# Kernel tuning notes

Hardware: AMD Instinct MI355X
Metric: run time of the kernel (lower is better)

Reference implementation:

```python
import jax, jax.numpy as jnp
import numpy as np

N = 40000
E = 640000
IN = 1300
H = 4
C = 64
G = 64  # number of graphs in the batch
NEG_SLOPE = 0.2


def gat_conv(x, edge_index, W, att_src, att_dst, bias):
    """PyG-style GATConv with default add_self_loops=True, concat heads.
    x: [N, F_in], W: [F_in, H*C], att_src/att_dst: [H, C], bias: [H*C].
    edge_index[0]=source j, edge_index[1]=target i (messages flow j->i).
    """
    n = x.shape[0]
    h = (x @ W).reshape(n, H, C)                      # [N, H, C]
    loop = jnp.arange(n, dtype=edge_index.dtype)
    src = jnp.concatenate([edge_index[0], loop])      # [E+N]
    dst = jnp.concatenate([edge_index[1], loop])      # [E+N]
    a_src = jnp.einsum('nhc,hc->nh', h, att_src)      # [N, H]
    a_dst = jnp.einsum('nhc,hc->nh', h, att_dst)      # [N, H]
    e = jax.nn.leaky_relu(a_src[src] + a_dst[dst], NEG_SLOPE)  # [E+N, H]
    # segment softmax over incoming edges of each target node
    e_max = jax.ops.segment_max(e, dst, num_segments=n)
    e = jnp.exp(e - e_max[dst])
    denom = jax.ops.segment_sum(e, dst, num_segments=n)
    alpha = e / (denom[dst] + 1e-16)                  # [E+N, H]
    msg = h[src] * alpha[:, :, None]                  # [E+N, H, C]
    out = jax.ops.segment_sum(msg, dst, num_segments=n)  # [N, H, C]
    return out.reshape(n, H * C) + bias


def global_mean_pool(x, batch, num_graphs):
    s = jax.ops.segment_sum(x, batch, num_segments=num_graphs)
    cnt = jax.ops.segment_sum(jnp.ones((x.shape[0],), x.dtype), batch,
                              num_segments=num_graphs)
    return s / jnp.maximum(cnt, 1.0)[:, None]


def setup_inputs() -> dict:
    key = jax.random.key(0)
    ks = jax.random.split(key, 12)
    x = jax.random.normal(ks[0], (N, IN), dtype=jnp.float32)
    edge_index = jax.random.randint(ks[1], (2, E), 0, N, dtype=jnp.int64)
    batch = jnp.sort(jax.random.randint(ks[2], (N,), 0, G, dtype=jnp.int64))
    s1 = 1.0 / np.sqrt(IN)
    s2 = 1.0 / np.sqrt(H * C)
    W1 = jax.random.normal(ks[3], (IN, H * C), dtype=jnp.float32) * s1
    att_src1 = jax.random.normal(ks[4], (H, C), dtype=jnp.float32) * s2
    att_dst1 = jax.random.normal(ks[5], (H, C), dtype=jnp.float32) * s2
    b1 = jnp.zeros((H * C,), jnp.float32)
    W2 = jax.random.normal(ks[6], (H * C, H * C), dtype=jnp.float32) * s2
    att_src2 = jax.random.normal(ks[7], (H, C), dtype=jnp.float32) * s2
    att_dst2 = jax.random.normal(ks[8], (H, C), dtype=jnp.float32) * s2
    b2 = jnp.zeros((H * C,), jnp.float32)
    lin_w = jax.random.normal(ks[9], (H * C, 1), dtype=jnp.float32) * s2
    lin_b = jnp.zeros((1,), jnp.float32)
    return {"x": x, "edge_index": edge_index, "batch": batch,
            "W1": W1, "att_src1": att_src1, "att_dst1": att_dst1, "b1": b1,
            "W2": W2, "att_src2": att_src2, "att_dst2": att_dst2, "b2": b2,
            "lin_w": lin_w, "lin_b": lin_b}


def reference(x, edge_index, batch, W1, att_src1, att_dst1, b1,
              W2, att_src2, att_dst2, b2, lin_w, lin_b):
    h = jax.nn.relu(gat_conv(x, edge_index, W1, att_src1, att_dst1, b1))
    h = jax.nn.relu(gat_conv(h, edge_index, W2, att_src2, att_dst2, b2))
    p = global_mean_pool(h, batch, G)                 # [G, H*C]
    out = p @ lin_w + lin_b                           # [G, 1]
    return out.squeeze()                              # [G]
```

## Files before the change

kernel.cpp:

```cpp
#include <hip/hip_runtime.h>
#include <hip/hip_bf16.h>

#define N_NODES 40000
#define N_EDGES 640000
#define F_IN    1300
#define NH      4
#define NC      64
#define F_OUT   256
#define NG      64
#define NEG_SLOPE 0.2f

typedef short short8v __attribute__((ext_vector_type(8)));
typedef float f32x16  __attribute__((ext_vector_type(16)));

__device__ __forceinline__ float lrelu(float x) { return x >= 0.f ? x : NEG_SLOPE * x; }

__device__ __forceinline__ short f2bf(float v) {
    unsigned u = __builtin_bit_cast(unsigned, v);
    unsigned r = (u + 0x7fffu + ((u >> 16) & 1u)) >> 16;
    return (short)r;
}
__device__ __forceinline__ float bf2f(short s) {
    unsigned u = ((unsigned)(unsigned short)s) << 16;
    return __builtin_bit_cast(float, u);
}

__device__ __forceinline__ short8v ld8(const short* p) {
    short4 a = *(const short4*)(p);
    short4 b = *(const short4*)(p + 4);
    short8v r;
    r[0] = a.x; r[1] = a.y; r[2] = a.z; r[3] = a.w;
    r[4] = b.x; r[5] = b.y; r[6] = b.z; r[7] = b.w;
    return r;
}

__global__ void wsplit_kernel(const float* __restrict__ W, short* __restrict__ hi,
                              short* __restrict__ lo, int K, int Kp)
{
    int idx = blockIdx.x * 256 + threadIdx.x;
    if (idx >= F_OUT * Kp) return;
    int n = idx / Kp, k = idx - n * Kp;
    float v = (k < K) ? W[(size_t)k * F_OUT + n] : 0.f;
    short h = f2bf(v);
    short l = f2bf(v - bf2f(h));
    hi[idx] = h;
    lo[idx] = l;
}

#define BK  32
#define BMR 32
#define LDK 36

__global__ __launch_bounds__(256, 4) void gemm_mfma_kernel(
    const float* __restrict__ A, const short* __restrict__ Bth,
    const short* __restrict__ Btl, float* __restrict__ C, int K, int Kp)
{
    __shared__ short As_hi[2][BMR][LDK];
    __shared__ short As_lo[2][BMR][LDK];

    const int t    = threadIdx.x;
    const int lane = t & 63;
    const int wv   = t >> 6;
    const int wc   = wv * 64;
    const int bm   = blockIdx.x * BMR;

    f32x16 acc[2];
#pragma unroll
    for (int j = 0; j < 2; ++j)
#pragma unroll
        for (int r = 0; r < 16; ++r) acc[j][r] = 0.f;

    const int arow = t >> 3;
    const int ac   = (t & 7) * 4;
    const int mr   = lane & 31;
    const int khalf = (lane >> 5) * 8;

    const size_t abase = (size_t)(bm + arow) * K;
    const size_t b0 = (size_t)(wc + mr) * Kp + khalf;
    const size_t b1 = (size_t)(wc + 32 + mr) * Kp + khalf;

    const int nt = Kp / BK;

    float4 av = make_float4(0.f, 0.f, 0.f, 0.f);
    if (ac < K) av = *(const float4*)&A[abase + ac];

    for (int it = 0; it < nt; ++it) {
        const int k0  = it * BK;
        const int buf = it & 1;

        const short8v bh0_0 = *(const short8v*)&Bth[b0 + k0];
        const short8v bh0_1 = *(const short8v*)&Bth[b0 + k0 + 16];
        const short8v bh1_0 = *(const short8v*)&Bth[b1 + k0];
        const short8v bh1_1 = *(const short8v*)&Bth[b1 + k0 + 16];
        const short8v bl0_0 = *(const short8v*)&Btl[b0 + k0];
        const short8v bl0_1 = *(const short8v*)&Btl[b0 + k0 + 16];
        const short8v bl1_0 = *(const short8v*)&Btl[b1 + k0];
        const short8v bl1_1 = *(const short8v*)&Btl[b1 + k0 + 16];

        {
            short4 h4, l4;
            h4.x = f2bf(av.x); l4.x = f2bf(av.x - bf2f(h4.x));
            h4.y = f2bf(av.y); l4.y = f2bf(av.y - bf2f(h4.y));
            h4.z = f2bf(av.z); l4.z = f2bf(av.z - bf2f(h4.z));
            h4.w = f2bf(av.w); l4.w = f2bf(av.w - bf2f(h4.w));
            *(short4*)&As_hi[buf][arow][ac] = h4;
            *(short4*)&As_lo[buf][arow][ac] = l4;
        }

        __syncthreads();
        __builtin_amdgcn_sched_barrier(0);

        float4 nv = make_float4(0.f, 0.f, 0.f, 0.f);
        if (it + 1 < nt) {
            int gk = k0 + BK + ac;
            if (gk < K) nv = *(const float4*)&A[abase + gk];
        }

#pragma unroll
        for (int ks = 0; ks < 2; ++ks) {
            const int ko = ks * 16 + khalf;
            short8v ah = ld8(&As_hi[buf][mr][ko]);
            short8v al = ld8(&As_lo[buf][mr][ko]);
            const short8v bh0 = ks ? bh0_1 : bh0_0;
            const short8v bh1 = ks ? bh1_1 : bh1_0;
            const short8v bl0 = ks ? bl0_1 : bl0_0;
            const short8v bl1 = ks ? bl1_1 : bl1_0;
            acc[0] = __builtin_amdgcn_mfma_f32_32x32x16_bf16(ah, bh0, acc[0], 0, 0, 0);
            acc[0] = __builtin_amdgcn_mfma_f32_32x32x16_bf16(ah, bl0, acc[0], 0, 0, 0);
            acc[0] = __builtin_amdgcn_mfma_f32_32x32x16_bf16(al, bh0, acc[0], 0, 0, 0);
            acc[1] = __builtin_amdgcn_mfma_f32_32x32x16_bf16(ah, bh1, acc[1], 0, 0, 0);
            acc[1] = __builtin_amdgcn_mfma_f32_32x32x16_bf16(ah, bl1, acc[1], 0, 0, 0);
            acc[1] = __builtin_amdgcn_mfma_f32_32x32x16_bf16(al, bh1, acc[1], 0, 0, 0);
        }
        av = nv;
    }
#pragma unroll
    for (int fn = 0; fn < 2; ++fn)
#pragma unroll
        for (int r = 0; r < 16; ++r) {
            int row = bm + (r & 3) + 8 * (r >> 2) + 4 * (lane >> 5);
            int col = wc + fn * 32 + mr;
            C[(size_t)row * F_OUT + col] = acc[fn][r];
        }
}

__global__ __launch_bounds__(256) void attn_coef_kernel(const float* __restrict__ h,
                                                        const float* __restrict__ att_s,
                                                        const float* __restrict__ att_d,
                                                        float* __restrict__ a_s,
                                                        float* __restrict__ a_d)
{
    const int n = blockIdx.x;
    const int t = threadIdx.x;
    const int w = t >> 6;
    const int l = t & 63;
    float hv = h[(size_t)n * F_OUT + t];
    float vs = hv * att_s[t];
    float vd = hv * att_d[t];
#pragma unroll
    for (int o = 1; o < 64; o <<= 1) {
        vs += __shfl_xor(vs, o);
        vd += __shfl_xor(vd, o);
    }
    if (l == 0) {
        a_s[n * NH + w] = vs;
        a_d[n * NH + w] = vd;
    }
}

__global__ void hist_kernel(const int* __restrict__ ei, int* __restrict__ deg)
{
    int e = blockIdx.x * blockDim.x + threadIdx.x;
    if (e < N_EDGES) atomicAdd(&deg[ei[N_EDGES + e]], 1);
}

__global__ __launch_bounds__(1024) void scan_kernel(const int* __restrict__ deg,
                                                    int* __restrict__ rowptr)
{
    __shared__ int sums[1024];
    const int t = threadIdx.x;
    const int chunk = (N_NODES + 1023) / 1024;
    int beg = t * chunk;
    int end = beg + chunk; if (end > N_NODES) end = N_NODES;
    if (beg > N_NODES) beg = N_NODES;
    int s = 0;
    for (int i = beg; i < end; ++i) s += deg[i];
    sums[t] = s;
    __syncthreads();
    for (int o = 1; o < 1024; o <<= 1) {
        int v = (t >= o) ? sums[t - o] : 0;
        __syncthreads();
        sums[t] += v;
        __syncthreads();
    }
    int run = (t == 0) ? 0 : sums[t - 1];
    for (int i = beg; i < end; ++i) { rowptr[i] = run; run += deg[i]; }
    if (t == 1023) rowptr[N_NODES] = run;
}

__global__ void scatter_kernel(const int* __restrict__ ei, int* __restrict__ cursor,
                               int* __restrict__ ssrc, int* __restrict__ edst)
{
    int e = blockIdx.x * blockDim.x + threadIdx.x;
    if (e < N_EDGES) {
        int d = ei[N_EDGES + e];
        int pos = atomicAdd(&cursor[d], 1);
        ssrc[pos] = ei[e];
        edst[pos] = d;
    }
}

__global__ void edge_logit_kernel(const int* __restrict__ ssrc,
                                  const int* __restrict__ edst,
                                  const float* __restrict__ a_s,
                                  const float* __restrict__ a_d,
                                  float* __restrict__ e_csr)
{
    int p = blockIdx.x * 256 + threadIdx.x;
    if (p >= N_EDGES) return;
    int s = ssrc[p], d = edst[p];
    float4 as = ((const float4*)a_s)[s];
    float4 ad = ((const float4*)a_d)[d];
    float4 e;
    e.x = lrelu(as.x + ad.x);
    e.y = lrelu(as.y + ad.y);
    e.z = lrelu(as.z + ad.z);
    e.w = lrelu(as.w + ad.w);
    ((float4*)e_csr)[p] = e;
}

__global__ __launch_bounds__(256) void agg_kernel(const float* __restrict__ h,
                                                  const float* __restrict__ e_csr,
                                                  const float* __restrict__ a_s,
                                                  const float* __restrict__ a_d,
                                                  const int* __restrict__ rowptr,
                                                  const int* __restrict__ ssrc,
                                                  const float* __restrict__ bias,
                                                  float* __restrict__ out)
{
    const int wv = threadIdx.x >> 6;
    const int n  = blockIdx.x * 4 + wv;
    const int l  = threadIdx.x & 63;

    const int beg = rowptr[n];
    const int deg = rowptr[n + 1] - beg;

    const int hA = l & 3;
    const float es = lrelu(a_s[n * NH + hA] + a_d[n * NH + hA]);
    const float* ep = e_csr + (size_t)beg * 4;

    float mx = es;
    for (int base = 0; base < deg; base += 16) {
        int i = base + (l >> 2);
        float e = (i < deg) ? ep[(size_t)i * 4 + hA] : -1e30f;
        mx = fmaxf(mx, e);
    }
#pragma unroll
    for (int o = 4; o < 64; o <<= 1) mx = fmaxf(mx, __shfl_xor(mx, o));

    float sm = ((l >> 2) == 0) ? __expf(es - mx) : 0.f;
    for (int base = 0; base < deg; base += 16) {
        int i = base + (l >> 2);
        sm += (i < deg) ? __expf(ep[(size_t)i * 4 + hA] - mx) : 0.f;
    }
#pragma unroll
    for (int o = 4; o < 64; o <<= 1) sm += __shfl_xor(sm, o);
    const float dinv = 1.f / (sm + 1e-16f);

    const int hB = l >> 4;
    const float mxB = __shfl(mx, hB);
    const float dvB = __shfl(dinv, hB);
    const float esB = __shfl(es, hB);

    const float4* h4 = (const float4*)h;
    float4 acc;
    {
        float sa = __expf(esB - mxB) * dvB;
        float4 hv = h4[(size_t)n * 64 + l];
        acc.x = sa * hv.x; acc.y = sa * hv.y; acc.z = sa * hv.z; acc.w = sa * hv.w;
    }
    int i = 0;
    for (; i + 8 <= deg; i += 8) {
        const int p = beg + i;
        int   s[8]; float e[8]; float4 v[8];
#pragma unroll
        for (int j = 0; j < 8; ++j) s[j] = ssrc[p + j];
#pragma unroll
        for (int j = 0; j < 8; ++j) e[j] = e_csr[(size_t)(p + j) * 4 + hB];
#pragma unroll
        for (int j = 0; j < 8; ++j) v[j] = h4[(size_t)s[j] * 64 + l];
#pragma unroll
        for (int j = 0; j < 8; ++j) {
            float a = __expf(e[j] - mxB) * dvB;
            acc.x += a * v[j].x; acc.y += a * v[j].y;
            acc.z += a * v[j].z; acc.w += a * v[j].w;
        }
    }
    for (; i < deg; ++i) {
        const int p = beg + i;
        int sj = ssrc[p];
        float a = __expf(e_csr[(size_t)p * 4 + hB] - mxB) * dvB;
        float4 hv = h4[(size_t)sj * 64 + l];
        acc.x += a * hv.x; acc.y += a * hv.y; acc.z += a * hv.z; acc.w += a * hv.w;
    }
    float4 bv = ((const float4*)bias)[l];
    float4 ov;
    ov.x = fmaxf(acc.x + bv.x, 0.f);
    ov.y = fmaxf(acc.y + bv.y, 0.f);
    ov.z = fmaxf(acc.z + bv.z, 0.f);
    ov.w = fmaxf(acc.w + bv.w, 0.f);
    ((float4*)out)[(size_t)n * 64 + l] = ov;
}

__global__ void ghist_kernel(const int* __restrict__ batch, int* __restrict__ gcnt)
{
    int n = blockIdx.x * blockDim.x + threadIdx.x;
    if (n < N_NODES) atomicAdd(&gcnt[batch[n]], 1);
}

__global__ __launch_bounds__(256) void pool_kernel(const float* __restrict__ x,
                                                   const int* __restrict__ gcnt,
                                                   const float* __restrict__ lin_w,
                                                   const float* __restrict__ lin_b,
                                                   float* __restrict__ out)
{
    const int g = blockIdx.x;
    const int t = threadIdx.x;
    __shared__ int s_start;
    if (t == 0) {
        int s = 0;
        for (int i = 0; i < g; ++i) s += gcnt[i];
        s_start = s;
    }
    __syncthreads();
    const int start = s_start;
    const int cnt = gcnt[g];
    float acc = 0.f;
    for (int i = 0; i < cnt; ++i) acc += x[(size_t)(start + i) * F_OUT + t];
    float p = acc / fmaxf((float)cnt, 1.f);
    float v = p * lin_w[t];
    __shared__ float red[256];
    red[t] = v;
    __syncthreads();
    for (int o = 128; o > 0; o >>= 1) {
        if (t < o) red[t] += red[t + o];
        __syncthreads();
    }
    if (t == 0) out[g] = red[0] + lin_b[0];
}

extern "C" void kernel_launch(void* const* d_in, const int* in_sizes, int n_in,
                              void* d_out, int out_size, void* d_ws, size_t ws_size,
                              hipStream_t stream)
{
    const float* x      = (const float*)d_in[0];
    const int*   ei     = (const int*)  d_in[1];
    const int*   batch  = (const int*)  d_in[2];
    const float* W1     = (const float*)d_in[3];
    const float* att_s1 = (const float*)d_in[4];
    const float* att_d1 = (const float*)d_in[5];
    const float* b1     = (const float*)d_in[6];
    const float* W2     = (const float*)d_in[7];
    const float* att_s2 = (const float*)d_in[8];
    const float* att_d2 = (const float*)d_in[9];
    const float* b2     = (const float*)d_in[10];
    const float* lin_w  = (const float*)d_in[11];
    const float* lin_b  = (const float*)d_in[12];
    float* out = (float*)d_out;

    const int Kp1 = 1312;
    const int Kp2 = 256;

    size_t off = 0;
    auto carve = [&](size_t bytes) -> void* {
        void* p = (char*)d_ws + off;
        off += (bytes + 255) & ~(size_t)255;
        return p;
    };
    float* hA     = (float*)carve((size_t)N_NODES * F_OUT * 4);
    float* hB     = (float*)carve((size_t)N_NODES * F_OUT * 4);
    float* a_s    = (float*)carve((size_t)N_NODES * NH * 4);
    float* a_d    = (float*)carve((size_t)N_NODES * NH * 4);
    int*   deg    = (int*)  carve((size_t)(N_NODES + 1) * 4);
    int*   rowptr = (int*)  carve((size_t)(N_NODES + 1) * 4);
    int*   cursor = (int*)  carve((size_t)N_NODES * 4);
    int*   ssrc   = (int*)  carve((size_t)N_EDGES * 4);
    int*   edst   = (int*)  carve((size_t)N_EDGES * 4);
    float* e_csr  = (float*)carve((size_t)N_EDGES * NH * 4);
    int*   gcnt   = (int*)  carve((size_t)NG * 4);
    short* Bt1h   = (short*)carve((size_t)F_OUT * Kp1 * 2);
    short* Bt1l   = (short*)carve((size_t)F_OUT * Kp1 * 2);
    short* Bt2h   = (short*)carve((size_t)F_OUT * Kp2 * 2);
    short* Bt2l   = (short*)carve((size_t)F_OUT * Kp2 * 2);
    (void)ws_size; (void)n_in; (void)in_sizes; (void)out_size;

    hipMemsetAsync(deg, 0, (size_t)(N_NODES + 1) * 4, stream);
    hipMemsetAsync(gcnt, 0, (size_t)NG * 4, stream);
    hist_kernel<<<(N_EDGES + 255) / 256, 256, 0, stream>>>(ei, deg);
    scan_kernel<<<1, 1024, 0, stream>>>(deg, rowptr);
    hipMemcpyAsync(cursor, rowptr, (size_t)N_NODES * 4, hipMemcpyDeviceToDevice, stream);
    scatter_kernel<<<(N_EDGES + 255) / 256, 256, 0, stream>>>(ei, cursor, ssrc, edst);
    ghist_kernel<<<(N_NODES + 255) / 256, 256, 0, stream>>>(batch, gcnt);
    wsplit_kernel<<<(F_OUT * Kp1 + 255) / 256, 256, 0, stream>>>(W1, Bt1h, Bt1l, F_IN, Kp1);
    wsplit_kernel<<<(F_OUT * Kp2 + 255) / 256, 256, 0, stream>>>(W2, Bt2h, Bt2l, F_OUT, Kp2);

    const int gblocks = N_NODES / BMR;
    const int ablocks = N_NODES / 4;
    const int eblocks = (N_EDGES + 255) / 256;

    gemm_mfma_kernel<<<gblocks, 256, 0, stream>>>(x, Bt1h, Bt1l, hA, F_IN, Kp1);
    attn_coef_kernel<<<N_NODES, 256, 0, stream>>>(hA, att_s1, att_d1, a_s, a_d);
    edge_logit_kernel<<<eblocks, 256, 0, stream>>>(ssrc, edst, a_s, a_d, e_csr);
    agg_kernel<<<ablocks, 256, 0, stream>>>(hA, e_csr, a_s, a_d, rowptr, ssrc, b1, hB);

    gemm_mfma_kernel<<<gblocks, 256, 0, stream>>>(hB, Bt2h, Bt2l, hA, F_OUT, Kp2);
    attn_coef_kernel<<<N_NODES, 256, 0, stream>>>(hA, att_s2, att_d2, a_s, a_d);
    edge_logit_kernel<<<eblocks, 256, 0, stream>>>(ssrc, edst, a_s, a_d, e_csr);
    agg_kernel<<<ablocks, 256, 0, stream>>>(hA, e_csr, a_s, a_d, rowptr, ssrc, b2, hB);

    pool_kernel<<<NG, 256, 0, stream>>>(hB, gcnt, lin_w, lin_b, out);
}
```

Baseline: 1.236 ms.

## Restage GEMM: share B tile in LDS, load A directly into registers

The GEMM now stages the bf16 hi/lo split weight tile (all 256 output columns) in double-buffered shared memory. A rows are read straight from global memory into MFMA operand registers and split to hi/lo on the fly. Each block now covers 64 rows with four waves, each wave handling 32x128, and launch bounds drop to 2 blocks per SM. The goal is to stop every wave from re-reading B out of global/L2 and to raise the MFMA work per load. The cost is more registers and shared memory, hence lower occupancy.

```diff
diff --git a/kernel.cpp b/kernel.cpp
--- a/kernel.cpp
+++ b/kernel.cpp
@@ -33,6 +33,26 @@
     r[4] = b.x; r[5] = b.y; r[6] = b.z; r[7] = b.w;
     return r;
 }
+__device__ __forceinline__ void st8(short* p, short8v v) {
+    short4 a, b;
+    a.x = v[0]; a.y = v[1]; a.z = v[2]; a.w = v[3];
+    b.x = v[4]; b.y = v[5]; b.z = v[6]; b.w = v[7];
+    *(short4*)(p)     = a;
+    *(short4*)(p + 4) = b;
+}
+
+__device__ __forceinline__ void cvt8(const float4 a, const float4 b,
+                                     short8v &h, short8v &l)
+{
+    h[0] = f2bf(a.x); l[0] = f2bf(a.x - bf2f(h[0]));
+    h[1] = f2bf(a.y); l[1] = f2bf(a.y - bf2f(h[1]));
+    h[2] = f2bf(a.z); l[2] = f2bf(a.z - bf2f(h[2]));
+    h[3] = f2bf(a.w); l[3] = f2bf(a.w - bf2f(h[3]));
+    h[4] = f2bf(b.x); l[4] = f2bf(b.x - bf2f(h[4]));
+    h[5] = f2bf(b.y); l[5] = f2bf(b.y - bf2f(h[5]));
+    h[6] = f2bf(b.z); l[6] = f2bf(b.z - bf2f(h[6]));
+    h[7] = f2bf(b.w); l[7] = f2bf(b.w - bf2f(h[7]));
+}
 
 __global__ void wsplit_kernel(const float* __restrict__ W, short* __restrict__ hi,
                               short* __restrict__ lo, int K, int Kp)
@@ -47,100 +67,149 @@
     lo[idx] = l;
 }
 
-#define BK  32
-#define BMR 32
-#define LDK 36
-
-__global__ __launch_bounds__(256, 4) void gemm_mfma_kernel(
+#define LDB 36
+
+__global__ __launch_bounds__(256, 2) void gemm_mfma_kernel(
     const float* __restrict__ A, const short* __restrict__ Bth,
     const short* __restrict__ Btl, float* __restrict__ C, int K, int Kp)
 {
-    __shared__ short As_hi[2][BMR][LDK];
-    __shared__ short As_lo[2][BMR][LDK];
-
-    const int t    = threadIdx.x;
-    const int lane = t & 63;
-    const int wv   = t >> 6;
-    const int wc   = wv * 64;
-    const int bm   = blockIdx.x * BMR;
-
-    f32x16 acc[2];
-#pragma unroll
-    for (int j = 0; j < 2; ++j)
+    __shared__ short Bs_hi[2][256][LDB];
+    __shared__ short Bs_lo[2][256][LDB];
+
+    const int t     = threadIdx.x;
+    const int lane  = t & 63;
+    const int wv    = t >> 6;
+    const int mr    = lane & 31;
+    const int khalf = (lane >> 5) * 8;
+    const int rbase = blockIdx.x * 64 + (wv >> 1) * 32;
+    const int cbase = (wv & 1) * 128;
+
+    f32x16 acc[4];
+#pragma unroll
+    for (int j = 0; j < 4; ++j)
 #pragma unroll
         for (int r = 0; r < 16; ++r) acc[j][r] = 0.f;
 
-    const int arow = t >> 3;
-    const int ac   = (t & 7) * 4;
-    const int mr   = lane & 31;
-    const int khalf = (lane >> 5) * 8;
-
-    const size_t abase = (size_t)(bm + arow) * K;
-    const size_t b0 = (size_t)(wc + mr) * Kp + khalf;
-    const size_t b1 = (size_t)(wc + 32 + mr) * Kp + khalf;
-
-    const int nt = Kp / BK;
-
-    float4 av = make_float4(0.f, 0.f, 0.f, 0.f);
-    if (ac < K) av = *(const float4*)&A[abase + ac];
+    const int nt = Kp / 32;
+    const size_t arow = (size_t)(rbase + mr) * K;
+    const size_t bcol = (size_t)t * Kp;
+
+    auto loadA8 = [&](int kg, float4 &x, float4 &y) {
+        if (kg + 8 <= K) {
+            x = *(const float4*)&A[arow + kg];
+            y = *(const float4*)&A[arow + kg + 4];
+        } else {
+            float v0 = (kg + 0 < K) ? A[arow + kg + 0] : 0.f;
+            float v1 = (kg + 1 < K) ? A[arow + kg + 1] : 0.f;
+            float v2 = (kg + 2 < K) ? A[arow + kg + 2] : 0.f;
+            float v3 = (kg + 3 < K) ? A[arow + kg + 3] : 0.f;
+            float v4 = (kg + 4 < K) ? A[arow + kg + 4] : 0.f;
+            float v5 = (kg + 5 < K) ? A[arow + kg + 5] : 0.f;
+            float v6 = (kg + 6 < K) ? A[arow + kg + 6] : 0.f;
+            float v7 = (kg + 7 < K) ? A[arow + kg + 7] : 0.f;
+            x = make_float4(v0, v1, v2, v3);
+            y = make_float4(v4, v5, v6, v7);
+        }
+    };
+
+    short8v pbh0, pbh1, pbh2, pbh3, pbl0, pbl1, pbl2, pbl3;
+    pbh0 = *(const short8v*)&Bth[bcol + 0];
+    pbh1 = *(const short8v*)&Bth[bcol + 8];
+    pbh2 = *(const short8v*)&Bth[bcol + 16];
+    pbh3 = *(const short8v*)&Bth[bcol + 24];
+    pbl0 = *(const short8v*)&Btl[bcol + 0];
+    pbl1 = *(const short8v*)&Btl[bcol + 8];
+    pbl2 = *(const short8v*)&Btl[bcol + 16];
+    pbl3 = *(const short8v*)&Btl[bcol + 24];
+    float4 a0x, a0y, a1x, a1y;
+    loadA8(khalf, a0x, a0y);
+    loadA8(16 + khalf, a1x, a1y);
+    st8(&Bs_hi[0][t][0],  pbh0);
+    st8(&Bs_hi[0][t][8],  pbh1);
+    st8(&Bs_hi[0][t][16], pbh2);
+    st8(&Bs_hi[0][t][24], pbh3);
+    st8(&Bs_lo[0][t][0],  pbl0);
+    st8(&Bs_lo[0][t][8],  pbl1);
+    st8(&Bs_lo[0][t][16], pbl2);
+    st8(&Bs_lo[0][t][24], pbl3);
+    asm volatile("s_waitcnt lgkmcnt(0)" ::: "memory");
+    __builtin_amdgcn_sched_barrier(0);
+    __builtin_amdgcn_s_barrier();
 
     for (int it = 0; it < nt; ++it) {
-        const int k0  = it * BK;
-        const int buf = it & 1;
-
-        const short8v bh0_0 = *(const short8v*)&Bth[b0 + k0];
-        const short8v bh0_1 = *(const short8v*)&Bth[b0 + k0 + 16];
-        const short8v bh1_0 = *(const short8v*)&Bth[b1 + k0];
-        const short8v bh1_1 = *(const short8v*)&Bth[b1 + k0 + 16];
-        const short8v bl0_0 = *(const short8v*)&Btl[b0 + k0];
-        const short8v bl0_1 = *(const short8v*)&Btl[b0 + k0 + 16];
-        const short8v bl1_0 = *(const short8v*)&Btl[b1 + k0];
-        const short8v bl1_1 = *(const short8v*)&Btl[b1 + k0 + 16];
+        const int buf  = it & 1;
+        const bool more = (it + 1 < nt);
+        const int k0n  = (it + 1) * 32;
+
+        short8v nbh0, nbh1, nbh2, nbh3, nbl0, nbl1, nbl2, nbl3;
+        float4 na0x, na0y, na1x, na1y;
+        if (more) {
+            nbh0 = *(const short8v*)&Bth[bcol + k0n + 0];
+            nbh1 = *(const short8v*)&Bth[bcol + k0n + 8];
+            nbh2 = *(const short8v*)&Bth[bcol + k0n + 16];
+            nbh3 = *(const short8v*)&Bth[bcol + k0n + 24];
+            nbl0 = *(const short8v*)&Btl[bcol + k0n + 0];
+            nbl1 = *(const short8v*)&Btl[bcol + k0n + 8];
+            nbl2 = *(const short8v*)&Btl[bcol + k0n + 16];
+            nbl3 = *(const short8v*)&Btl[bcol + k0n + 24];
+            loadA8(k0n + khalf, na0x, na0y);
+            loadA8(k0n + 16 + khalf, na1x, na1y);
+        } else {
+            nbh0 = nbh1 = nbh2 = nbh3 = (short8v)0;
+            nbl0 = nbl1 = nbl2 = nbl3 = (short8v)0;
+            na0x = na0y = na1x = na1y = make_float4(0.f, 0.f, 0.f, 0.f);
+        }
 
         {
-            short4 h4, l4;
-            h4.x = f2bf(av.x); l4.x = f2bf(av.x - bf2f(h4.x));
-            h4.y = f2bf(av.y); l4.y = f2bf(av.y - bf2f(h4.y));
-            h4.z = f2bf(av.z); l4.z = f2bf(av.z - bf2f(h4.z));
-            h4.w = f2bf(av.w); l4.w = f2bf(av.w - bf2f(h4.w));
-            *(short4*)&As_hi[buf][arow][ac] = h4;
-            *(short4*)&As_lo[buf][arow][ac] = l4;
-        }
-
-        __syncthreads();
+            short8v ah, al;
+            cvt8(a0x, a0y, ah, al);
+#pragma unroll
+            for (int cf = 0; cf < 4; ++cf) {
+                const short* ph = &Bs_hi[buf][cbase + cf * 32 + mr][khalf];
+                const short* pl = &Bs_lo[buf][cbase + cf * 32 + mr][khalf];
+                short8v bh = ld8(ph);
+                short8v bl = ld8(pl);
+                acc[cf] = __builtin_amdgcn_mfma_f32_32x32x16_bf16(ah, bh, acc[cf], 0, 0, 0);
+                acc[cf] = __builtin_amdgcn_mfma_f32_32x32x16_bf16(ah, bl, acc[cf], 0, 0, 0);
+                acc[cf] = __builtin_amdgcn_mfma_f32_32x32x16_bf16(al, bh, acc[cf], 0, 0, 0);
+            }
+            cvt8(a1x, a1y, ah, al);
+#pragma unroll
+            for (int cf = 0; cf < 4; ++cf) {
+                const short* ph = &Bs_hi[buf][cbase + cf * 32 + mr][16 + khalf];
+                const short* pl = &Bs_lo[buf][cbase + cf * 32 + mr][16 + khalf];
+                short8v bh = ld8(ph);
+                short8v bl = ld8(pl);
+                acc[cf] = __builtin_amdgcn_mfma_f32_32x32x16_bf16(ah, bh, acc[cf], 0, 0, 0);
+                acc[cf] = __builtin_amdgcn_mfma_f32_32x32x16_bf16(ah, bl, acc[cf], 0, 0, 0);
+                acc[cf] = __builtin_amdgcn_mfma_f32_32x32x16_bf16(al, bh, acc[cf], 0, 0, 0);
+            }
+        }
+
+        if (more) {
+            st8(&Bs_hi[buf ^ 1][t][0],  nbh0);
+            st8(&Bs_hi[buf ^ 1][t][8],  nbh1);
+            st8(&Bs_hi[buf ^ 1][t][16], nbh2);
+            st8(&Bs_hi[buf ^ 1][t][24], nbh3);
+            st8(&Bs_lo[buf ^ 1][t][0],  nbl0);
+            st8(&Bs_lo[buf ^ 1][t][8],  nbl1);
+            st8(&Bs_lo[buf ^ 1][t][16], nbl2);
+            st8(&Bs_lo[buf ^ 1][t][24], nbl3);
+        }
+        asm volatile("s_waitcnt lgkmcnt(0)" ::: "memory");
         __builtin_amdgcn_sched_barrier(0);
-
-        float4 nv = make_float4(0.f, 0.f, 0.f, 0.f);
-        if (it + 1 < nt) {
-            int gk = k0 + BK + ac;
-            if (gk < K) nv = *(const float4*)&A[abase + gk];
-        }
-
-#pragma unroll
-        for (int ks = 0; ks < 2; ++ks) {
-            const int ko = ks * 16 + khalf;
-            short8v ah = ld8(&As_hi[buf][mr][ko]);
-            short8v al = ld8(&As_lo[buf][mr][ko]);
-            const short8v bh0 = ks ? bh0_1 : bh0_0;
-            const short8v bh1 = ks ? bh1_1 : bh1_0;
-            const short8v bl0 = ks ? bl0_1 : bl0_0;
-            const short8v bl1 = ks ? bl1_1 : bl1_0;
-            acc[0] = __builtin_amdgcn_mfma_f32_32x32x16_bf16(ah, bh0, acc[0], 0, 0, 0);
-            acc[0] = __builtin_amdgcn_mfma_f32_32x32x16_bf16(ah, bl0, acc[0], 0, 0, 0);
-            acc[0] = __builtin_amdgcn_mfma_f32_32x32x16_bf16(al, bh0, acc[0], 0, 0, 0);
-            acc[1] = __builtin_amdgcn_mfma_f32_32x32x16_bf16(ah, bh1, acc[1], 0, 0, 0);
-            acc[1] = __builtin_amdgcn_mfma_f32_32x32x16_bf16(ah, bl1, acc[1], 0, 0, 0);
-            acc[1] = __builtin_amdgcn_mfma_f32_32x32x16_bf16(al, bh1, acc[1], 0, 0, 0);
-        }
-        av = nv;
-    }
-#pragma unroll
-    for (int fn = 0; fn < 2; ++fn)
+        __builtin_amdgcn_s_barrier();
+
+        a0x = na0x; a0y = na0y; a1x = na1x; a1y = na1y;
+    }
+
+#pragma unroll
+    for (int cf = 0; cf < 4; ++cf)
 #pragma unroll
         for (int r = 0; r < 16; ++r) {
-            int row = bm + (r & 3) + 8 * (r >> 2) + 4 * (lane >> 5);
-            int col = wc + fn * 32 + mr;
-            C[(size_t)row * F_OUT + col] = acc[fn][r];
+            int row = rbase + (r & 3) + 8 * (r >> 2) + 4 * (lane >> 5);
+            int col = cbase + cf * 32 + mr;
+            C[(size_t)row * F_OUT + col] = acc[cf][r];
         }
 }
 
@@ -404,7 +473,7 @@
     wsplit_kernel<<<(F_OUT * Kp1 + 255) / 256, 256, 0, stream>>>(W1, Bt1h, Bt1l, F_IN, Kp1);
     wsplit_kernel<<<(F_OUT * Kp2 + 255) / 256, 256, 0, stream>>>(W2, Bt2h, Bt2l, F_OUT, Kp2);
 
-    const int gblocks = N_NODES / BMR;
+    const int gblocks = N_NODES / 64;
     const int ablocks = N_NODES / 4;
     const int eblocks = (N_EDGES + 255) / 256;
 
```

Result: faster. 1.208 ms (-2.2%).
